# Kernel optimization log

Measured on AMD Instinct MI355X. Metric: run time of the kernel, lower is better.

## Reference

```python
import jax, jax.numpy as jnp
import numpy as np

A, M, H = 4, 1024, 1024
E, N = 8, 4096

def setup_inputs() -> dict:
    key = jax.random.key(0)
    kx, k1, k2 = jax.random.split(key, 3)
    x = jax.random.normal(kx, (A, M, H), dtype=jnp.float32)
    w1 = jax.random.normal(k1, (E, H, N), dtype=jnp.float32) * 0.02
    w2 = jax.random.normal(k2, (E, N, H), dtype=jnp.float32) * 0.02
    return {"x": x, "w1": w1, "w2": w2}

def reference(x, w1, w2):
    # mid: [A, E, M, N] = up-projection per expert
    mid = jnp.einsum('amh,ehn->aemn', x, w1)
    # down-projection per expert, then sum over experts e
    out = jnp.einsum('aemn,enh->amh', mid, w2)
    return out
```

## Files before the change

### kernel.cpp

```cpp
#include <hip/hip_runtime.h>
#include <hip/hip_bf16.h>
#include <stdint.h>


#define BN 128

typedef __attribute__((ext_vector_type(8))) short short8;
typedef __attribute__((ext_vector_type(4))) float float4v;
typedef __attribute__((ext_vector_type(4))) unsigned int uint4v;

__device__ __forceinline__ unsigned int rne_hi(unsigned int u) {
  return u + 0x7fffu + ((u >> 16) & 1u);
}

__device__ __forceinline__ unsigned int pack_bf16(float lo, float hi) {
  unsigned int ulo = rne_hi(__float_as_uint(lo));
  unsigned int uhi = rne_hi(__float_as_uint(hi));
  return __builtin_amdgcn_perm(uhi, ulo, 0x07060302u);
}

__device__ __forceinline__ void load_lds_16B(const void* g, void* lds) {
  __builtin_amdgcn_global_load_lds(
      (__attribute__((address_space(1))) void*)(uintptr_t)g,
      (__attribute__((address_space(3))) void*)(unsigned int)(uintptr_t)lds,
      16, 0, 0);
}


template <int MH, int NH>
__device__ __forceinline__ void mma_ph(float4v acc[8][4], const short8* aR,
                                       const short8 bR[2][4]) {
  __builtin_amdgcn_s_setprio(1);
#pragma unroll
  for (int fi = 0; fi < 4; ++fi)
#pragma unroll
    for (int fj = 0; fj < 2; ++fj)
#pragma unroll
      for (int s = 0; s < 2; ++s)
        acc[MH * 4 + fi][NH * 2 + fj] = __builtin_amdgcn_mfma_f32_16x16x32_bf16(
            aR[fi * 2 + s], bR[NH][fj * 2 + s], acc[MH * 4 + fi][NH * 2 + fj],
            0, 0, 0);
  __builtin_amdgcn_s_setprio(0);
}

__global__ __launch_bounds__(512, 2) void gemm1_8ph(
    const unsigned short* __restrict__ A, const unsigned short* __restrict__ Bt,
    float* __restrict__ C, long expStride, int ld, int Kc, int zdiv) {
  __shared__ __attribute__((aligned(16))) unsigned short As[2][2][128 * 64];
  __shared__ __attribute__((aligned(16))) unsigned short Bs[2][2][128 * 64];

  const int tid = threadIdx.x;
  const int wv = tid >> 6;
  const int ln = tid & 63;
  const int lrow = ln & 15;
  const int lq = ln >> 4;
  const int wmh = wv >> 2;
  const int wnq = wv & 3;
  const int breg = wnq >> 1;
  const int brow0 = (wnq & 1) * 64;

  const int nwg = gridDim.x;
  int wg = blockIdx.x;
  if ((nwg & 7) == 0) wg = (wg & 7) * (nwg >> 3) + (wg >> 3);
  const int tile = wg & 15;
  const int z = wg >> 4;
  const int e = z / zdiv;
  const int kc = z % zdiv;
  const int ty = tile >> 2, tx = tile & 3;

  const unsigned short* Ab =
      A + (long)e * expStride + (long)(ty * 256) * ld + (long)kc * Kc;
  const unsigned short* Bb =
      Bt + (long)e * expStride + (long)(tx * 256) * ld + (long)kc * Kc;

  const int srow = ln >> 3;
  const int scg = (ln & 7) ^ srow;

  auto stageA = [&](int b, int h, int kt) {
#pragma unroll
    for (int i = 0; i < 2; ++i) {
      const unsigned short* g =
          Ab + (long)(h * 128 + wv * 16 + i * 8 + srow) * ld + kt * 64 + scg * 8;
      load_lds_16B(g, (void*)&As[b][h][(wv * 2 + i) * 512]);
    }
  };
  auto stageB = [&](int b, int h, int kt) {
#pragma unroll
    for (int i = 0; i < 2; ++i) {
      const unsigned short* g =
          Bb + (long)(h * 128 + wv * 16 + i * 8 + srow) * ld + kt * 64 + scg * 8;
      load_lds_16B(g, (void*)&Bs[b][h][(wv * 2 + i) * 512]);
    }
  };

  float4v acc[8][4];
  float4v zero4 = {0.0f, 0.0f, 0.0f, 0.0f};
#pragma unroll
  for (int i = 0; i < 8; ++i)
#pragma unroll
    for (int j = 0; j < 4; ++j) acc[i][j] = zero4;

  short8 aR[8];
  short8 bR[2][4];

  auto ldsA = [&](int b, int mh) {
#pragma unroll
    for (int fi = 0; fi < 4; ++fi) {
      const int row = mh * 64 + fi * 16 + lrow;
#pragma unroll
      for (int s = 0; s < 2; ++s) {
        const int cg = (s * 4 + lq) ^ (row & 7);
        aR[fi * 2 + s] = *(const short8*)&As[b][wmh][row * 64 + cg * 8];
      }
    }
  };
  auto ldsB = [&](int b, int nh) {
#pragma unroll
    for (int fj = 0; fj < 2; ++fj) {
      const int row = brow0 + nh * 32 + fj * 16 + lrow;
#pragma unroll
      for (int s = 0; s < 2; ++s) {
        const int cg = (s * 4 + lq) ^ (row & 7);
        bR[nh][fj * 2 + s] = *(const short8*)&Bs[b][breg][row * 64 + cg * 8];
      }
    }
  };

  const int nkt = Kc / 64;

  stageA(0, 0, 0);
  stageA(0, 1, 0);
  stageB(0, 0, 0);
  stageB(0, 1, 0);
  stageB(1, 0, 1);
  stageB(1, 1, 1);
  asm volatile("s_waitcnt vmcnt(4)" ::: "memory");
  __builtin_amdgcn_s_barrier();

#define HALF_ITER(B, OB, NN)                                        \
  {                                                                 \
    const int na = ((NN) + 1 < nkt) ? (NN) + 1 : nkt - 1;           \
    const int nb = ((NN) + 2 < nkt) ? (NN) + 2 : nkt - 1;           \
    ldsA(B, 0);                                                     \
    ldsB(B, 0);                                                     \
    stageA(OB, 0, na);                                              \
    __builtin_amdgcn_s_barrier();                                   \
    asm volatile("s_waitcnt lgkmcnt(0)");                           \
    mma_ph<0, 0>(acc, aR, bR);                                      \
    __builtin_amdgcn_s_barrier();                                   \
    ldsB(B, 1);                                                     \
    stageA(OB, 1, na);                                              \
    __builtin_amdgcn_s_barrier();                                   \
    asm volatile("s_waitcnt lgkmcnt(0)");                           \
    mma_ph<0, 1>(acc, aR, bR);                                      \
    __builtin_amdgcn_s_barrier();                                   \
    ldsA(B, 1);                                                     \
    stageB(B, 0, nb);                                               \
    __builtin_amdgcn_s_barrier();                                   \
    asm volatile("s_waitcnt lgkmcnt(0)");                           \
    mma_ph<1, 1>(acc, aR, bR);                                      \
    __builtin_amdgcn_s_barrier();                                   \
    stageB(B, 1, nb);                                               \
    __builtin_amdgcn_s_barrier();                                   \
    mma_ph<1, 0>(acc, aR, bR);                                      \
    asm volatile("s_waitcnt vmcnt(4)" ::: "memory");                \
    __builtin_amdgcn_s_barrier();                                   \
  }

  for (int t = 0; t < nkt; t += 2) {
    HALF_ITER(0, 1, t)
    HALF_ITER(1, 0, t + 1)
  }
#undef HALF_ITER

  asm volatile("s_waitcnt vmcnt(0)" ::: "memory");

  const int crow0 = ty * 256 + wmh * 128 + lq * 4;
  const int ccol0 = tx * 256 + wnq * 64 + lrow;
#pragma unroll
  for (int i = 0; i < 8; ++i)
#pragma unroll
    for (int j = 0; j < 4; ++j)
#pragma unroll
      for (int r = 0; r < 4; ++r)
        atomicAdd(&C[(long)(crow0 + i * 16 + r) * 1024 + ccol0 + j * 16],
                  acc[i][j][r]);
}

template <int MI, bool ATOMIC>
__global__ __launch_bounds__(256) void gemm_bf16(
    const unsigned short* __restrict__ A, int lda, long strideA,
    const unsigned short* __restrict__ Bt, int ldb, long strideB,
    float* __restrict__ C, int ldc, int K, int zdiv) {
  constexpr int BM = MI * 32;
  __shared__ __attribute__((aligned(16))) unsigned short As[2 * BM * 32];
  __shared__ __attribute__((aligned(16))) unsigned short Bs[2 * BN * 32];

  const int tid = threadIdx.x;
  const int wv = tid >> 6;
  const int ln = tid & 63;
  const int wm = (wv >> 1) * (MI * 16);
  const int wn = (wv & 1) * 64;
  const int lrow = ln & 15;
  const int lq = ln >> 4;
  const int sfrag = ((lq + (lrow >> 1)) & 3) * 16;

  const int zb = blockIdx.z / zdiv;
  const int zk = blockIdx.z % zdiv;
  const unsigned short* Ab = A + (long)zb * strideA + (long)zk * K +
                             (long)(blockIdx.y * BM) * lda;
  const unsigned short* Bb = Bt + (long)zb * strideB + (long)zk * K +
                             (long)(blockIdx.x * BN) * ldb;

  float4v zero4 = {0.0f, 0.0f, 0.0f, 0.0f};
  float4v acc[MI][4];
#pragma unroll
  for (int i = 0; i < MI; ++i)
#pragma unroll
    for (int j = 0; j < 4; ++j) acc[i][j] = zero4;

  const int nk = K / 64;
  for (int kt = 0; kt < nk; ++kt) {
    const int k0 = kt * 64;
    __syncthreads();
#pragma unroll
    for (int s = 0; s < 2; ++s) {
#pragma unroll
      for (int p = 0; p < BM / 64; ++p) {
        int o = p * 256 + wv * 64 + ln;
        int r = o >> 2;
        int gk = ((o & 3) - (r >> 1)) & 3;
        const unsigned short* g = Ab + (long)r * lda + k0 + s * 32 + gk * 8;
        char* lp = (char*)As + s * (BM * 64) + (p * 256 + wv * 64) * 16;
        load_lds_16B(g, lp);
      }
#pragma unroll
      for (int p = 0; p < 2; ++p) {
        int o = p * 256 + wv * 64 + ln;
        int r = o >> 2;
        int gk = ((o & 3) - (r >> 1)) & 3;
        const unsigned short* g = Bb + (long)r * ldb + k0 + s * 32 + gk * 8;
        char* lp = (char*)Bs + s * (BN * 64) + (p * 256 + wv * 64) * 16;
        load_lds_16B(g, lp);
      }
    }
    __syncthreads();

#pragma unroll
    for (int s = 0; s < 2; ++s) {
      short8 a[MI], b[4];
#pragma unroll
      for (int i = 0; i < MI; ++i)
        a[i] = *(const short8*)((const char*)As + s * (BM * 64) +
                                (wm + i * 16 + lrow) * 64 + sfrag);
#pragma unroll
      for (int j = 0; j < 4; ++j)
        b[j] = *(const short8*)((const char*)Bs + s * (BN * 64) +
                                (wn + j * 16 + lrow) * 64 + sfrag);
#pragma unroll
      for (int i = 0; i < MI; ++i)
#pragma unroll
        for (int j = 0; j < 4; ++j)
          acc[i][j] = __builtin_amdgcn_mfma_f32_16x16x32_bf16(a[i], b[j],
                                                              acc[i][j], 0, 0, 0);
    }
  }

  const int crow0 = blockIdx.y * BM + wm + lq * 4;
  const int ccol0 = blockIdx.x * BN + wn + lrow;
#pragma unroll
  for (int i = 0; i < MI; ++i)
#pragma unroll
    for (int j = 0; j < 4; ++j)
#pragma unroll
      for (int r = 0; r < 4; ++r) {
        int row = crow0 + i * 16 + r;
        int col = ccol0 + j * 16;
        if (ATOMIC)
          atomicAdd(&C[(long)row * ldc + col], acc[i][j][r]);
        else
          C[(long)row * ldc + col] = acc[i][j][r];
      }
}

__global__ __launch_bounds__(256) void cvt_f32_bf16(
    const float* __restrict__ in, unsigned short* __restrict__ out) {
  long i = ((long)blockIdx.x * 256 + threadIdx.x) * 8;
  float4 v0 = *(const float4*)(in + i);
  float4 v1 = *(const float4*)(in + i + 4);
  uint4v d;
  d.x = pack_bf16(v0.x, v0.y);
  d.y = pack_bf16(v0.z, v0.w);
  d.z = pack_bf16(v1.x, v1.y);
  d.w = pack_bf16(v1.z, v1.w);
  *(uint4v*)(out + i) = d;
}

__global__ __launch_bounds__(256) void transpose_cvt_kernel(
    const float* __restrict__ in, unsigned short* __restrict__ out,
    int R, int C, long strideBatch) {
  __shared__ float tile[64][65];
  const float* src = in + (long)blockIdx.z * strideBatch;
  unsigned short* dst = out + (long)blockIdx.z * strideBatch;
  const int t = threadIdx.x;
  const int c4 = (t & 15) * 4;
  const int r0 = t >> 4;
  const int by = blockIdx.y * 64;
  const int bx = blockIdx.x * 64;
#pragma unroll
  for (int p = 0; p < 4; ++p) {
    int r = r0 + p * 16;
    float4 v = *(const float4*)(src + (long)(by + r) * C + bx + c4);
    tile[r][c4 + 0] = v.x;
    tile[r][c4 + 1] = v.y;
    tile[r][c4 + 2] = v.z;
    tile[r][c4 + 3] = v.w;
  }
  __syncthreads();
#pragma unroll
  for (int p = 0; p < 4; ++p) {
    int cc = r0 + p * 16;
    int rr = c4;
    unsigned int d0 = pack_bf16(tile[rr + 0][cc], tile[rr + 1][cc]);
    unsigned int d1 = pack_bf16(tile[rr + 2][cc], tile[rr + 3][cc]);
    uint2 dd;
    dd.x = d0;
    dd.y = d1;
    *(uint2*)(dst + (long)(bx + cc) * R + by + rr) = dd;
  }
}

extern "C" void kernel_launch(void* const* d_in, const int* in_sizes, int n_in,
                              void* d_out, int out_size, void* d_ws, size_t ws_size,
                              hipStream_t stream) {
  const float* x = (const float*)d_in[0];
  const float* w1 = (const float*)d_in[1];
  const float* w2 = (const float*)d_in[2];
  float* out = (float*)d_out;

  const int A_ = 4, M_ = 1024, H_ = 1024, E_ = 8, N_ = 4096;
  const long EXP = (long)H_ * N_;

  const size_t need_single =
      (size_t)2 * E_ * EXP * 2 + (size_t)A_ * M_ * H_ * 2 +
      (size_t)H_ * H_ * 4 + (size_t)H_ * H_ * 2;

  if (ws_size >= need_single) {
    unsigned short* w2t = (unsigned short*)d_ws;
    unsigned short* w1b = w2t + (long)E_ * EXP;
    unsigned short* xb = w1b + (long)E_ * EXP;
    float* Wacc = (float*)(xb + (long)A_ * M_ * H_);
    unsigned short* Wb = (unsigned short*)(Wacc + (long)H_ * H_);

    cvt_f32_bf16<<<(A_ * M_ * H_) / 2048, 256, 0, stream>>>(x, xb);
    transpose_cvt_kernel<<<dim3(H_ / 64, N_ / 64, E_), 256, 0, stream>>>(
        w2, w2t, N_, H_, EXP);
    cvt_f32_bf16<<<(int)(E_ * EXP / 2048), 256, 0, stream>>>(w1, w1b);
    hipMemsetAsync(Wacc, 0, (size_t)H_ * H_ * 4, stream);

    gemm1_8ph<<<dim3(256), 512, 0, stream>>>(w2t, w1b, Wacc, EXP, N_, N_ / 2, 2);

    cvt_f32_bf16<<<(H_ * H_) / 2048, 256, 0, stream>>>(Wacc, Wb);

    gemm_bf16<2, false><<<dim3(H_ / BN, (A_ * M_) / 64, 1), 256, 0, stream>>>(
        xb, H_, 0, Wb, H_, 0, out, H_, H_, 1);
  } else {
    unsigned short* w2t = (unsigned short*)d_ws;
    unsigned short* w1b = w2t + 4 * EXP;
    unsigned short* xb = w1b + 4 * EXP;
    float* Wacc = (float*)(xb + (long)A_ * M_ * H_);
    unsigned short* Wb = (unsigned short*)(Wacc + (long)H_ * H_);

    cvt_f32_bf16<<<(A_ * M_ * H_) / 2048, 256, 0, stream>>>(x, xb);
    hipMemsetAsync(Wacc, 0, (size_t)H_ * H_ * 4, stream);

    for (int g = 0; g < 2; ++g) {
      const float* w2g = w2 + (long)g * 4 * EXP;
      const float* w1g = w1 + (long)g * 4 * EXP;
      transpose_cvt_kernel<<<dim3(H_ / 64, N_ / 64, 4), 256, 0, stream>>>(
          w2g, w2t, N_, H_, EXP);
      cvt_f32_bf16<<<(int)(4 * EXP / 2048), 256, 0, stream>>>(w1g, w1b);
      gemm1_8ph<<<dim3(256), 512, 0, stream>>>(w2t, w1b, Wacc, EXP, N_, N_ / 4, 4);
    }

    cvt_f32_bf16<<<(H_ * H_) / 2048, 256, 0, stream>>>(Wacc, Wb);
    gemm_bf16<2, false><<<dim3(H_ / BN, (A_ * M_) / 64, 1), 256, 0, stream>>>(
        xb, H_, 0, Wb, H_, 0, out, H_, H_, 1);
  }
}
```

Baseline: 427.2 us.

## Replace atomic split-K accumulation with partial buffers and deepen A prefetch

The weight-product GEMM now writes each split-K slice's result to its own partial buffer instead of using float atomicAdd. A new kernel sums the 16 partials and converts the total to bf16, which also removes the memset and the separate convert launch. The main loop is also restaged so that both A and B tiles are prefetched two k-steps ahead, with the vmcnt wait raised to match. This costs an extra 64 MB of workspace traffic for the partials and the reduction, and it raises the number of outstanding loads.

```diff
diff --git a/kernel.cpp b/kernel.cpp
--- a/kernel.cpp
+++ b/kernel.cpp
@@ -43,6 +43,7 @@
   __builtin_amdgcn_s_setprio(0);
 }
 
+template <bool ATOMIC>
 __global__ __launch_bounds__(512, 2) void gemm1_8ph(
     const unsigned short* __restrict__ A, const unsigned short* __restrict__ Bt,
     float* __restrict__ C, long expStride, int ld, int Kc, int zdiv) {
@@ -132,49 +133,51 @@
   stageA(0, 1, 0);
   stageB(0, 0, 0);
   stageB(0, 1, 0);
+  stageA(1, 0, 1);
+  stageA(1, 1, 1);
   stageB(1, 0, 1);
   stageB(1, 1, 1);
-  asm volatile("s_waitcnt vmcnt(4)" ::: "memory");
+  asm volatile("s_waitcnt vmcnt(8)" ::: "memory");
   __builtin_amdgcn_s_barrier();
 
-#define HALF_ITER(B, OB, NN)                                        \
+#define HALF_ITER(B, NN)                                            \
   {                                                                 \
-    const int na = ((NN) + 1 < nkt) ? (NN) + 1 : nkt - 1;           \
-    const int nb = ((NN) + 2 < nkt) ? (NN) + 2 : nkt - 1;           \
+    const int n2 = ((NN) + 2 < nkt) ? (NN) + 2 : nkt - 1;           \
     ldsA(B, 0);                                                     \
     ldsB(B, 0);                                                     \
-    stageA(OB, 0, na);                                              \
     __builtin_amdgcn_s_barrier();                                   \
     asm volatile("s_waitcnt lgkmcnt(0)");                           \
     mma_ph<0, 0>(acc, aR, bR);                                      \
     __builtin_amdgcn_s_barrier();                                   \
     ldsB(B, 1);                                                     \
-    stageA(OB, 1, na);                                              \
     __builtin_amdgcn_s_barrier();                                   \
     asm volatile("s_waitcnt lgkmcnt(0)");                           \
     mma_ph<0, 1>(acc, aR, bR);                                      \
     __builtin_amdgcn_s_barrier();                                   \
     ldsA(B, 1);                                                     \
-    stageB(B, 0, nb);                                               \
+    stageB(B, 0, n2);                                               \
+    stageB(B, 1, n2);                                               \
     __builtin_amdgcn_s_barrier();                                   \
     asm volatile("s_waitcnt lgkmcnt(0)");                           \
     mma_ph<1, 1>(acc, aR, bR);                                      \
     __builtin_amdgcn_s_barrier();                                   \
-    stageB(B, 1, nb);                                               \
+    stageA(B, 0, n2);                                               \
+    stageA(B, 1, n2);                                               \
     __builtin_amdgcn_s_barrier();                                   \
     mma_ph<1, 0>(acc, aR, bR);                                      \
-    asm volatile("s_waitcnt vmcnt(4)" ::: "memory");                \
+    asm volatile("s_waitcnt vmcnt(8)" ::: "memory");                \
     __builtin_amdgcn_s_barrier();                                   \
   }
 
   for (int t = 0; t < nkt; t += 2) {
-    HALF_ITER(0, 1, t)
-    HALF_ITER(1, 0, t + 1)
+    HALF_ITER(0, t)
+    HALF_ITER(1, t + 1)
   }
 #undef HALF_ITER
 
   asm volatile("s_waitcnt vmcnt(0)" ::: "memory");
 
+  float* Cz = ATOMIC ? C : C + (long)z * (1024L * 1024L);
   const int crow0 = ty * 256 + wmh * 128 + lq * 4;
   const int ccol0 = tx * 256 + wnq * 64 + lrow;
 #pragma unroll
@@ -182,9 +185,31 @@
 #pragma unroll
     for (int j = 0; j < 4; ++j)
 #pragma unroll
-      for (int r = 0; r < 4; ++r)
-        atomicAdd(&C[(long)(crow0 + i * 16 + r) * 1024 + ccol0 + j * 16],
-                  acc[i][j][r]);
+      for (int r = 0; r < 4; ++r) {
+        const long idx = (long)(crow0 + i * 16 + r) * 1024 + ccol0 + j * 16;
+        if (ATOMIC)
+          atomicAdd(&Cz[idx], acc[i][j][r]);
+        else
+          Cz[idx] = acc[i][j][r];
+      }
+}
+
+__global__ __launch_bounds__(256) void reduce16_cvt(
+    const float* __restrict__ in, unsigned short* __restrict__ out) {
+  const long i = ((long)blockIdx.x * 256 + threadIdx.x) * 4;
+  float4 s = *(const float4*)(in + i);
+#pragma unroll
+  for (int zz = 1; zz < 16; ++zz) {
+    float4 v = *(const float4*)(in + (long)zz * (1024L * 1024L) + i);
+    s.x += v.x;
+    s.y += v.y;
+    s.z += v.z;
+    s.w += v.w;
+  }
+  uint2 d;
+  d.x = pack_bf16(s.x, s.y);
+  d.y = pack_bf16(s.z, s.w);
+  *(uint2*)(out + i) = d;
 }
 
 template <int MI, bool ATOMIC>
@@ -341,11 +366,29 @@
   const int A_ = 4, M_ = 1024, H_ = 1024, E_ = 8, N_ = 4096;
   const long EXP = (long)H_ * N_;
 
-  const size_t need_single =
-      (size_t)2 * E_ * EXP * 2 + (size_t)A_ * M_ * H_ * 2 +
-      (size_t)H_ * H_ * 4 + (size_t)H_ * H_ * 2;
-
-  if (ws_size >= need_single) {
+  const size_t base = (size_t)2 * E_ * EXP * 2 + (size_t)A_ * M_ * H_ * 2;
+  const size_t need_part = base + 16ull * H_ * H_ * 4 + (size_t)H_ * H_ * 2;
+  const size_t need_single = base + (size_t)H_ * H_ * 4 + (size_t)H_ * H_ * 2;
+
+  if (ws_size >= need_part) {
+    unsigned short* w2t = (unsigned short*)d_ws;
+    unsigned short* w1b = w2t + (long)E_ * EXP;
+    unsigned short* xb = w1b + (long)E_ * EXP;
+    float* Wpart = (float*)(xb + (long)A_ * M_ * H_);
+    unsigned short* Wb = (unsigned short*)(Wpart + 16L * H_ * H_);
+
+    cvt_f32_bf16<<<(A_ * M_ * H_) / 2048, 256, 0, stream>>>(x, xb);
+    transpose_cvt_kernel<<<dim3(H_ / 64, N_ / 64, E_), 256, 0, stream>>>(
+        w2, w2t, N_, H_, EXP);
+    cvt_f32_bf16<<<(int)(E_ * EXP / 2048), 256, 0, stream>>>(w1, w1b);
+
+    gemm1_8ph<false><<<dim3(256), 512, 0, stream>>>(w2t, w1b, Wpart, EXP, N_,
+                                                    N_ / 2, 2);
+    reduce16_cvt<<<(H_ * H_) / 1024, 256, 0, stream>>>(Wpart, Wb);
+
+    gemm_bf16<2, false><<<dim3(H_ / BN, (A_ * M_) / 64, 1), 256, 0, stream>>>(
+        xb, H_, 0, Wb, H_, 0, out, H_, H_, 1);
+  } else if (ws_size >= need_single) {
     unsigned short* w2t = (unsigned short*)d_ws;
     unsigned short* w1b = w2t + (long)E_ * EXP;
     unsigned short* xb = w1b + (long)E_ * EXP;
@@ -358,8 +401,8 @@
     cvt_f32_bf16<<<(int)(E_ * EXP / 2048), 256, 0, stream>>>(w1, w1b);
     hipMemsetAsync(Wacc, 0, (size_t)H_ * H_ * 4, stream);
 
-    gemm1_8ph<<<dim3(256), 512, 0, stream>>>(w2t, w1b, Wacc, EXP, N_, N_ / 2, 2);
-
+    gemm1_8ph<true><<<dim3(256), 512, 0, stream>>>(w2t, w1b, Wacc, EXP, N_,
+                                                   N_ / 2, 2);
     cvt_f32_bf16<<<(H_ * H_) / 2048, 256, 0, stream>>>(Wacc, Wb);
 
     gemm_bf16<2, false><<<dim3(H_ / BN, (A_ * M_) / 64, 1), 256, 0, stream>>>(
@@ -380,7 +423,8 @@
       transpose_cvt_kernel<<<dim3(H_ / 64, N_ / 64, 4), 256, 0, stream>>>(
           w2g, w2t, N_, H_, EXP);
       cvt_f32_bf16<<<(int)(4 * EXP / 2048), 256, 0, stream>>>(w1g, w1b);
-      gemm1_8ph<<<dim3(256), 512, 0, stream>>>(w2t, w1b, Wacc, EXP, N_, N_ / 4, 4);
+      gemm1_8ph<true><<<dim3(256), 512, 0, stream>>>(w2t, w1b, Wacc, EXP, N_,
+                                                     N_ / 4, 4);
     }
 
     cvt_f32_bf16<<<(H_ * H_) / 2048, 256, 0, stream>>>(Wacc, Wb);
```

Result: faster. 402.6 us (-5.8%).
